# Kernel tuning notes

Measured on AMD Instinct MI355X. Metric: run time of the kernel, lower is better.

## Reference

```python
import jax, jax.numpy as jnp
import numpy as np

NUM_EMBEDDINGS = 512
EMBEDDING_DIM = 256
COMMITMENT_COST = 0.25


def setup_inputs() -> dict:
    key = jax.random.key(0)
    k1, k2 = jax.random.split(key)
    z = jax.random.normal(k1, (8, EMBEDDING_DIM, 16, 32, 32), dtype=jnp.float32)
    # codebook initialized uniform(-1/K, 1/K) like the torch module
    e = jax.random.uniform(k2, (NUM_EMBEDDINGS, EMBEDDING_DIM), dtype=jnp.float32,
                           minval=-1.0 / NUM_EMBEDDINGS, maxval=1.0 / NUM_EMBEDDINGS)
    return {"z": z, "e": e}


def reference(z, e):
    B, D, T, h, w = z.shape
    K = e.shape[0]
    # [B,D,T,h,w] -> [N, D]
    z_flat = jnp.transpose(z, (0, 2, 3, 4, 1)).reshape(-1, D)
    # squared L2 distances to codebook: [N, K]
    d = (jnp.sum(z_flat ** 2, axis=1, keepdims=True)
         + jnp.sum(e ** 2, axis=1)
         - 2.0 * z_flat @ e.T)
    idx = jnp.argmin(d, axis=1)                      # [N] int
    z_q_raw = e[idx].reshape(B, T, h, w, D)          # codebook gather
    z_q_raw = jnp.transpose(z_q_raw, (0, 4, 1, 2, 3))  # [B,D,T,h,w]

    commit = jnp.mean((jax.lax.stop_gradient(z_q_raw) - z) ** 2)
    codebk = jnp.mean((z_q_raw - jax.lax.stop_gradient(z)) ** 2)
    vq_loss = codebk + COMMITMENT_COST * commit

    # straight-through estimator
    z_q = z + jax.lax.stop_gradient(z_q_raw - z)

    # perplexity: histogram of code usage (avoids materializing NxK one-hot)
    N = idx.shape[0]
    avg_probs = jnp.zeros((K,), z.dtype).at[idx].add(1.0) / N
    perplexity = jnp.exp(-jnp.sum(avg_probs * jnp.log(avg_probs + 1e-10)))

    return z_q, vq_loss, idx, perplexity
```

## Files before the change

### kernel.cpp

```cpp
#include <hip/hip_runtime.h>
#include <math.h>

#define N_POS     131072
#define DIM       256
#define K_CODES   512
#define S_SPATIAL 16384
#define ZQ_ELEMS  33554432
#define OUT_LOSS  33554432
#define OUT_IDXB  33554433
#define OUT_PERP  (33554433 + 131072)

#define WS_LOSS   0
#define WS_HIST   16
#define WS_E2     2064
#define WS_FIXED  2064

__global__ __launch_bounds__(256) void e2_kernel(const float* __restrict__ e,
                                                 float* __restrict__ e2) {
    int k = blockIdx.x * 256 + threadIdx.x;
    if (k >= K_CODES) return;
    const float* row = e + (size_t)k * DIM;
    float half[2];
#pragma unroll
    for (int h = 0; h < 2; ++h) {
        const float* base = row + h * 128;
        float r[8];
#pragma unroll
        for (int j = 0; j < 8; ++j) {
            float v = base[j];
            r[j] = __fmul_rn(v, v);
        }
        for (int i = 8; i < 128; i += 8) {
#pragma unroll
            for (int j = 0; j < 8; ++j) {
                float v = base[i + j];
                r[j] = __fadd_rn(r[j], __fmul_rn(v, v));
            }
        }
        half[h] = __fadd_rn(__fadd_rn(__fadd_rn(r[0], r[1]), __fadd_rn(r[2], r[3])),
                            __fadd_rn(__fadd_rn(r[4], r[5]), __fadd_rn(r[6], r[7])));
    }
    e2[k] = __fadd_rn(half[0], half[1]);
}

__global__ __launch_bounds__(256) void transpose_e(const float* __restrict__ e,
                                                   float* __restrict__ eTq) {
    int t = blockIdx.x * 256 + threadIdx.x;
    int k = t >> 8;
    int d = t & 255;
    float v = e[t];
    int c = k >> 6;
    int l = k & 63;
    eTq[(d << 9) + (l << 3) + c] = v;
}

__global__ __launch_bounds__(256) void sz_kernel(const float* __restrict__ z,
                                                 float* __restrict__ sz) {
    int n = blockIdx.x * 256 + threadIdx.x;
    int b = n >> 14;
    int s = n & (S_SPATIAL - 1);
    const float* zp = z + (size_t)b * (DIM * S_SPATIAL) + s;
    float half[2];
#pragma unroll
    for (int h = 0; h < 2; ++h) {
        const float* base = zp + (size_t)(h * 128) * S_SPATIAL;
        float r[8];
#pragma unroll
        for (int j = 0; j < 8; ++j) {
            float v = base[(size_t)j * S_SPATIAL];
            r[j] = __fmul_rn(v, v);
        }
        for (int i = 8; i < 128; i += 8) {
#pragma unroll
            for (int j = 0; j < 8; ++j) {
                float v = base[(size_t)(i + j) * S_SPATIAL];
                r[j] = __fadd_rn(r[j], __fmul_rn(v, v));
            }
        }
        half[h] = __fadd_rn(__fadd_rn(__fadd_rn(r[0], r[1]), __fadd_rn(r[2], r[3])),
                            __fadd_rn(__fadd_rn(r[4], r[5]), __fadd_rn(r[6], r[7])));
    }
    sz[n] = __fadd_rn(half[0], half[1]);
}

__global__ __launch_bounds__(64, 2) void pass1_dist(const float* __restrict__ z,
                                                    const float* __restrict__ eTq,
                                                    const float* __restrict__ e2,
                                                    const float* __restrict__ sz,
                                                    float* __restrict__ idxf,
                                                    int* __restrict__ ghist) {
    const int lane = threadIdx.x;
    const int n0   = blockIdx.x << 4;
    const int b    = n0 >> 14;
    const float* zb = z + (size_t)b * (DIM * S_SPATIAL) + (n0 & (S_SPATIAL - 1));

    __shared__ float zs[DIM][16];

    for (int j = lane; j < 1024; j += 64) {
        int d  = j >> 2;
        int p4 = (j & 3) << 2;
        float4 v = *(const float4*)(zb + ((size_t)d << 14) + p4);
        *(float4*)(&zs[d][p4]) = v;
    }

    float szv = sz[n0 + (lane & 15)];

    float se[8];
#pragma unroll
    for (int c = 0; c < 8; ++c) se[c] = e2[(c << 6) + lane];

    float a0[16], a1[16], a2[16], a3[16], a4[16], a5[16], a6[16], a7[16];
#pragma unroll
    for (int p = 0; p < 16; ++p) {
        a0[p] = 0.f; a1[p] = 0.f; a2[p] = 0.f; a3[p] = 0.f;
        a4[p] = 0.f; a5[p] = 0.f; a6[p] = 0.f; a7[p] = 0.f;
    }

    __syncthreads();

    const float* ep = eTq + (lane << 3);

#define LOADZ(zv, d) do {                                        \
        *(float4*)((zv) +  0) = *(const float4*)(&zs[(d)][ 0]);  \
        *(float4*)((zv) +  4) = *(const float4*)(&zs[(d)][ 4]);  \
        *(float4*)((zv) +  8) = *(const float4*)(&zs[(d)][ 8]);  \
        *(float4*)((zv) + 12) = *(const float4*)(&zs[(d)][12]);  \
    } while (0)

#define LOADE(e0, e1, d) do {                                    \
        e0 = *(const float4*)(ep + ((size_t)(d) << 9));          \
        e1 = *(const float4*)(ep + ((size_t)(d) << 9) + 4);      \
    } while (0)

#define FMAS(zv, e0, e1) do {                                    \
        _Pragma("unroll")                                        \
        for (int p = 0; p < 16; ++p) {                           \
            float zp_ = (zv)[p];                                 \
            a0[p] = __fmaf_rn(zp_, (e0).x, a0[p]);               \
            a1[p] = __fmaf_rn(zp_, (e0).y, a1[p]);               \
            a2[p] = __fmaf_rn(zp_, (e0).z, a2[p]);               \
            a3[p] = __fmaf_rn(zp_, (e0).w, a3[p]);               \
            a4[p] = __fmaf_rn(zp_, (e1).x, a4[p]);               \
            a5[p] = __fmaf_rn(zp_, (e1).y, a5[p]);               \
            a6[p] = __fmaf_rn(zp_, (e1).z, a6[p]);               \
            a7[p] = __fmaf_rn(zp_, (e1).w, a7[p]);               \
        }                                                        \
    } while (0)

    float zvA[16], zvB[16];
    float4 eA0, eA1, eB0, eB1;
    LOADZ(zvA, 0); LOADE(eA0, eA1, 0);
    LOADZ(zvB, 1); LOADE(eB0, eB1, 1);
#pragma unroll 1
    for (int d = 0; d < DIM - 2; d += 2) {
        FMAS(zvA, eA0, eA1);
        LOADZ(zvA, d + 2); LOADE(eA0, eA1, d + 2);
        FMAS(zvB, eB0, eB1);
        LOADZ(zvB, d + 3); LOADE(eB0, eB1, d + 3);
    }
    FMAS(zvA, eA0, eA1);
    FMAS(zvB, eB0, eB1);

#undef LOADZ
#undef LOADE
#undef FMAS

    unsigned long long myMin = 0xffffffffffffffffull;
#pragma unroll
    for (int p = 0; p < 16; ++p) {
        float szp = __shfl(szv, p);
        float d0 = __fsub_rn(__fadd_rn(szp, se[0]), __fmul_rn(2.0f, a0[p]));
        float d1 = __fsub_rn(__fadd_rn(szp, se[1]), __fmul_rn(2.0f, a1[p]));
        float d2 = __fsub_rn(__fadd_rn(szp, se[2]), __fmul_rn(2.0f, a2[p]));
        float d3 = __fsub_rn(__fadd_rn(szp, se[3]), __fmul_rn(2.0f, a3[p]));
        float d4 = __fsub_rn(__fadd_rn(szp, se[4]), __fmul_rn(2.0f, a4[p]));
        float d5 = __fsub_rn(__fadd_rn(szp, se[5]), __fmul_rn(2.0f, a5[p]));
        float d6 = __fsub_rn(__fadd_rn(szp, se[6]), __fmul_rn(2.0f, a6[p]));
        float d7 = __fsub_rn(__fadd_rn(szp, se[7]), __fmul_rn(2.0f, a7[p]));
        unsigned long long k0 = ((unsigned long long)__float_as_uint(d0) << 32) | (unsigned int)(lane);
        unsigned long long k1 = ((unsigned long long)__float_as_uint(d1) << 32) | (unsigned int)(lane + 64);
        unsigned long long k2 = ((unsigned long long)__float_as_uint(d2) << 32) | (unsigned int)(lane + 128);
        unsigned long long k3 = ((unsigned long long)__float_as_uint(d3) << 32) | (unsigned int)(lane + 192);
        unsigned long long k4 = ((unsigned long long)__float_as_uint(d4) << 32) | (unsigned int)(lane + 256);
        unsigned long long k5 = ((unsigned long long)__float_as_uint(d5) << 32) | (unsigned int)(lane + 320);
        unsigned long long k6 = ((unsigned long long)__float_as_uint(d6) << 32) | (unsigned int)(lane + 384);
        unsigned long long k7 = ((unsigned long long)__float_as_uint(d7) << 32) | (unsigned int)(lane + 448);
        unsigned long long m01 = k1 < k0 ? k1 : k0;
        unsigned long long m23 = k3 < k2 ? k3 : k2;
        unsigned long long m45 = k5 < k4 ? k5 : k4;
        unsigned long long m67 = k7 < k6 ? k7 : k6;
        unsigned long long mA = m23 < m01 ? m23 : m01;
        unsigned long long mB = m67 < m45 ? m67 : m45;
        unsigned long long kmin = mB < mA ? mB : mA;
#pragma unroll
        for (int off = 32; off; off >>= 1) {
            unsigned long long o = __shfl_xor(kmin, off);
            kmin = o < kmin ? o : kmin;
        }
        if (lane == p) myMin = kmin;
    }
    if (lane < 16) {
        int idx = (int)(unsigned int)(myMin & 0xffffffffull);
        idxf[n0 + lane] = (float)idx;
        atomicAdd(&ghist[idx], 1);
    }
}

__global__ __launch_bounds__(256) void gather_loss(const float* __restrict__ z,
                                                   const float* __restrict__ e,
                                                   const float* __restrict__ idxf,
                                                   float* __restrict__ out,
                                                   double* __restrict__ loss) {
    int t = blockIdx.x * 256 + threadIdx.x;
    int b   = t >> 14;
    int r   = t & 16383;
    int dg  = r >> 12;
    int sp  = (r & 4095) << 2;
    int n0  = (b << 14) + sp;

    int k0 = (int)idxf[n0 + 0];
    int k1 = (int)idxf[n0 + 1];
    int k2 = (int)idxf[n0 + 2];
    int k3 = (int)idxf[n0 + 3];
    const float* e0 = e + (size_t)k0 * DIM;
    const float* e1 = e + (size_t)k1 * DIM;
    const float* e2p = e + (size_t)k2 * DIM;
    const float* e3 = e + (size_t)k3 * DIM;

    const float* zb = z + ((size_t)b * DIM << 14) + sp;
    float* ob = out + ((size_t)b * DIM << 14) + sp;

    double acc = 0.0;
    int dend = dg * 64 + 64;
    for (int d0 = dg * 64; d0 < dend; d0 += 4) {
        float4 ev0 = *(const float4*)(e0 + d0);
        float4 ev1 = *(const float4*)(e1 + d0);
        float4 ev2 = *(const float4*)(e2p + d0);
        float4 ev3 = *(const float4*)(e3 + d0);
#pragma unroll
        for (int dd = 0; dd < 4; ++dd) {
            size_t off = ((size_t)(d0 + dd) << 14);
            float4 zv = *(const float4*)(zb + off);
            float ea = (dd == 0) ? ev0.x : (dd == 1) ? ev0.y : (dd == 2) ? ev0.z : ev0.w;
            float eb_ = (dd == 0) ? ev1.x : (dd == 1) ? ev1.y : (dd == 2) ? ev1.z : ev1.w;
            float ec = (dd == 0) ? ev2.x : (dd == 1) ? ev2.y : (dd == 2) ? ev2.z : ev2.w;
            float ed = (dd == 0) ? ev3.x : (dd == 1) ? ev3.y : (dd == 2) ? ev3.z : ev3.w;
            float d0f = __fsub_rn(ea, zv.x);
            float d1f = __fsub_rn(eb_, zv.y);
            float d2f = __fsub_rn(ec, zv.z);
            float d3f = __fsub_rn(ed, zv.w);
            float4 ov;
            ov.x = __fadd_rn(zv.x, d0f);
            ov.y = __fadd_rn(zv.y, d1f);
            ov.z = __fadd_rn(zv.z, d2f);
            ov.w = __fadd_rn(zv.w, d3f);
            *(float4*)(ob + off) = ov;
            acc += (double)d0f * (double)d0f;
            acc += (double)d1f * (double)d1f;
            acc += (double)d2f * (double)d2f;
            acc += (double)d3f * (double)d3f;
        }
    }
    for (int off = 32; off; off >>= 1) acc += __shfl_down(acc, off);
    __shared__ double red[4];
    if ((threadIdx.x & 63) == 0) red[threadIdx.x >> 6] = acc;
    __syncthreads();
    if (threadIdx.x == 0) {
        double tsum = red[0] + red[1] + red[2] + red[3];
        atomicAdd(loss, tsum);
    }
}

__global__ __launch_bounds__(512) void finalize_kernel(const int* __restrict__ ghist,
                                                       const double* __restrict__ loss,
                                                       float* __restrict__ out) {
    int k = threadIdx.x;
    double p = (double)ghist[k] / (double)N_POS;
    double t = p * log(p + 1e-10);
    for (int off = 32; off; off >>= 1) t += __shfl_down(t, off);
    __shared__ double red[8];
    if ((k & 63) == 0) red[k >> 6] = t;
    __syncthreads();
    if (k == 0) {
        double sum = 0.0;
        for (int i = 0; i < 8; ++i) sum += red[i];
        double perp = exp(-sum);
        double mse  = (*loss) / (double)ZQ_ELEMS;
        out[OUT_LOSS] = (float)(1.25 * mse);
        out[OUT_PERP] = (float)perp;
    }
}

extern "C" void kernel_launch(void* const* d_in, const int* in_sizes, int n_in,
                              void* d_out, int out_size, void* d_ws, size_t ws_size,
                              hipStream_t stream) {
    const float* z = (const float*)d_in[0];
    const float* e = (const float*)d_in[1];
    float* out = (float*)d_out;
    char* ws = (char*)d_ws;

    double* loss  = (double*)(ws + WS_LOSS);
    int*    ghist = (int*)(ws + WS_HIST);
    float*  e2    = (float*)(ws + WS_E2);
    float*  idxf  = out + OUT_IDXB;

    float* eTq = (float*)d_out;
    float* szp = (float*)d_out + 131072;

    hipMemsetAsync(d_ws, 0, WS_FIXED, stream);

    e2_kernel      <<<2, 256, 0, stream>>>(e, e2);
    transpose_e    <<<512, 256, 0, stream>>>(e, eTq);
    sz_kernel      <<<N_POS / 256, 256, 0, stream>>>(z, szp);
    pass1_dist     <<<N_POS / 16, 64, 0, stream>>>(z, eTq, e2, szp, idxf, ghist);
    gather_loss    <<<N_POS / 256, 256, 0, stream>>>(z, e, idxf, out, loss);
    finalize_kernel<<<1, 512, 0, stream>>>(ghist, loss, out);
}
```

Before: 677.1 us.

## Load z tiles via scalar s_load into SGPRs instead of LDS staging

```diff
diff --git a/kernel.cpp b/kernel.cpp
--- a/kernel.cpp
+++ b/kernel.cpp
@@ -14,6 +14,8 @@
 #define WS_HIST   16
 #define WS_E2     2064
 #define WS_FIXED  2064
+
+typedef float sfloat16 __attribute__((ext_vector_type(16)));
 
 __global__ __launch_bounds__(256) void e2_kernel(const float* __restrict__ e,
                                                  float* __restrict__ e2) {
@@ -83,7 +85,7 @@
     sz[n] = __fadd_rn(half[0], half[1]);
 }
 
-__global__ __launch_bounds__(64, 2) void pass1_dist(const float* __restrict__ z,
+__global__ __launch_bounds__(64, 3) void pass1_dist(const float* __restrict__ z,
                                                     const float* __restrict__ eTq,
                                                     const float* __restrict__ e2,
                                                     const float* __restrict__ sz,
@@ -92,16 +94,9 @@
     const int lane = threadIdx.x;
     const int n0   = blockIdx.x << 4;
     const int b    = n0 >> 14;
-    const float* zb = z + (size_t)b * (DIM * S_SPATIAL) + (n0 & (S_SPATIAL - 1));
-
-    __shared__ float zs[DIM][16];
-
-    for (int j = lane; j < 1024; j += 64) {
-        int d  = j >> 2;
-        int p4 = (j & 3) << 2;
-        float4 v = *(const float4*)(zb + ((size_t)d << 14) + p4);
-        *(float4*)(&zs[d][p4]) = v;
-    }
+    const unsigned long long zbase =
+        (unsigned long long)(const void*)(z + (size_t)b * (DIM * S_SPATIAL)
+                                            + (n0 & (S_SPATIAL - 1)));
 
     float szv = sz[n0 + (lane & 15)];
 
@@ -116,53 +111,41 @@
         a4[p] = 0.f; a5[p] = 0.f; a6[p] = 0.f; a7[p] = 0.f;
     }
 
-    __syncthreads();
-
     const float* ep = eTq + (lane << 3);
-
-#define LOADZ(zv, d) do {                                        \
-        *(float4*)((zv) +  0) = *(const float4*)(&zs[(d)][ 0]);  \
-        *(float4*)((zv) +  4) = *(const float4*)(&zs[(d)][ 4]);  \
-        *(float4*)((zv) +  8) = *(const float4*)(&zs[(d)][ 8]);  \
-        *(float4*)((zv) + 12) = *(const float4*)(&zs[(d)][12]);  \
-    } while (0)
-
-#define LOADE(e0, e1, d) do {                                    \
-        e0 = *(const float4*)(ep + ((size_t)(d) << 9));          \
-        e1 = *(const float4*)(ep + ((size_t)(d) << 9) + 4);      \
-    } while (0)
 
 #define FMAS(zv, e0, e1) do {                                    \
         _Pragma("unroll")                                        \
         for (int p = 0; p < 16; ++p) {                           \
-            float zp_ = (zv)[p];                                 \
-            a0[p] = __fmaf_rn(zp_, (e0).x, a0[p]);               \
-            a1[p] = __fmaf_rn(zp_, (e0).y, a1[p]);               \
-            a2[p] = __fmaf_rn(zp_, (e0).z, a2[p]);               \
-            a3[p] = __fmaf_rn(zp_, (e0).w, a3[p]);               \
-            a4[p] = __fmaf_rn(zp_, (e1).x, a4[p]);               \
-            a5[p] = __fmaf_rn(zp_, (e1).y, a5[p]);               \
-            a6[p] = __fmaf_rn(zp_, (e1).z, a6[p]);               \
-            a7[p] = __fmaf_rn(zp_, (e1).w, a7[p]);               \
+            a0[p] = __fmaf_rn((zv)[p], (e0).x, a0[p]);           \
+            a1[p] = __fmaf_rn((zv)[p], (e0).y, a1[p]);           \
+            a2[p] = __fmaf_rn((zv)[p], (e0).z, a2[p]);           \
+            a3[p] = __fmaf_rn((zv)[p], (e0).w, a3[p]);           \
+            a4[p] = __fmaf_rn((zv)[p], (e1).x, a4[p]);           \
+            a5[p] = __fmaf_rn((zv)[p], (e1).y, a5[p]);           \
+            a6[p] = __fmaf_rn((zv)[p], (e1).z, a6[p]);           \
+            a7[p] = __fmaf_rn((zv)[p], (e1).w, a7[p]);           \
         }                                                        \
     } while (0)
 
-    float zvA[16], zvB[16];
-    float4 eA0, eA1, eB0, eB1;
-    LOADZ(zvA, 0); LOADE(eA0, eA1, 0);
-    LOADZ(zvB, 1); LOADE(eB0, eB1, 1);
 #pragma unroll 1
-    for (int d = 0; d < DIM - 2; d += 2) {
-        FMAS(zvA, eA0, eA1);
-        LOADZ(zvA, d + 2); LOADE(eA0, eA1, d + 2);
-        FMAS(zvB, eB0, eB1);
-        LOADZ(zvB, d + 3); LOADE(eB0, eB1, d + 3);
-    }
-    FMAS(zvA, eA0, eA1);
-    FMAS(zvB, eB0, eB1);
-
-#undef LOADZ
-#undef LOADE
+    for (int d = 0; d < DIM; d += 2) {
+        float4 e0 = *(const float4*)(ep + ((size_t)d << 9));
+        float4 e1 = *(const float4*)(ep + ((size_t)d << 9) + 4);
+        float4 f0 = *(const float4*)(ep + ((size_t)(d + 1) << 9));
+        float4 f1 = *(const float4*)(ep + ((size_t)(d + 1) << 9) + 4);
+
+        sfloat16 zA, zB;
+        unsigned long long addrA = zbase + ((unsigned long long)d << 16);
+        unsigned long long addrB = addrA + 65536ull;
+        asm volatile("s_load_dwordx16 %0, %2, 0x0\n\t"
+                     "s_load_dwordx16 %1, %3, 0x0\n\t"
+                     "s_waitcnt lgkmcnt(0)"
+                     : "=&s"(zA), "=&s"(zB)
+                     : "s"(addrA), "s"(addrB));
+
+        FMAS(zA, e0, e1);
+        FMAS(zB, f0, f1);
+    }
 #undef FMAS
 
     unsigned long long myMin = 0xffffffffffffffffull;
```

Result: faster. 627.5 us (-7.3%).
